# Kernel optimization log

Hardware: AMD Instinct MI355X
Metric: run time of the kernel (lower is better)

Reference implementation:

```python
import jax, jax.numpy as jnp
import numpy as np

N_QUBITS = 4
Q_DEPTH = 6
Q_DELTA = 0.01


def _conv1d(x, w, b):
    # x: (B, Cin, L), w: (Cout, Cin, 3), padding=1
    y = jax.lax.conv_general_dilated(x, w, window_strides=(1,), padding=[(1, 1)],
                                     dimension_numbers=('NCH', 'OIH', 'NCH'))
    return y + b[None, :, None]


def _maxpool2(x):
    B, C, L = x.shape
    return x.reshape(B, C, L // 2, 2).max(axis=-1)


def _take(state, i, axis):
    return jax.lax.index_in_dim(state, i, axis, keepdims=False)


def _apply_ry(state, theta, wire):
    # state: (B, 2, 2, 2, 2); theta: scalar (shared weight) or (B,) (per-sample)
    half = theta * 0.5
    c, s = jnp.cos(half), jnp.sin(half)
    if c.ndim == 1:  # per-sample angles -> broadcast over remaining qubit axes
        c = c.reshape(-1, 1, 1, 1)
        s = s.reshape(-1, 1, 1, 1)
    ax = wire + 1
    s0 = _take(state, 0, ax)
    s1 = _take(state, 1, ax)
    return jnp.stack([c * s0 - s * s1, s * s0 + c * s1], axis=ax)


def _apply_cnot(state, ctrl, tgt):
    cax, tax = ctrl + 1, tgt + 1
    a0 = jax.lax.slice_in_dim(state, 0, 1, axis=cax)
    a1 = jax.lax.slice_in_dim(state, 1, 2, axis=cax)
    return jnp.concatenate([a0, jnp.flip(a1, axis=tax)], axis=cax)


def _quantum_forward(q_in, q_params):
    # Batched 4-qubit state-vector simulation (PennyLane default.qubit semantics,
    # wire 0 = most significant -> axis wire+1 of (B,2,2,2,2) state).
    B = q_in.shape[0]
    # H layer on |0000> -> uniform amplitude 1/4
    state = jnp.full((B, 2, 2, 2, 2), 0.25, dtype=q_in.dtype)
    for w in range(N_QUBITS):
        state = _apply_ry(state, q_in[:, w], w)
    qw = q_params.reshape(Q_DEPTH, N_QUBITS)
    for k in range(Q_DEPTH):
        # entangling layer: CNOT(0,1), CNOT(2,3), then CNOT(1,2)
        state = _apply_cnot(state, 0, 1)
        state = _apply_cnot(state, 2, 3)
        state = _apply_cnot(state, 1, 2)
        for w in range(N_QUBITS):
            state = _apply_ry(state, qw[k, w], w)
    probs = state * state  # real amplitudes throughout (H as initial |+>^n, RY, CNOT)
    zs = [(_take(probs, 0, q + 1) - _take(probs, 1, q + 1)).sum(axis=(1, 2, 3))
          for q in range(N_QUBITS)]
    return jnp.stack(zs, axis=1)  # (B, 4) <Z_q>


def setup_inputs() -> dict:
    key = jax.random.key(0)
    ks = jax.random.split(key, 12)
    B, F = 32768, 64
    FLAT = 64 * (F // 4)  # 1024
    return {
        'x': jax.random.normal(ks[0], (B, F), jnp.float32),
        'conv1_w': jax.random.normal(ks[1], (32, 1, 3), jnp.float32) * 0.3,
        'conv1_b': jax.random.normal(ks[2], (32,), jnp.float32) * 0.05,
        'conv2_w': jax.random.normal(ks[3], (64, 32, 3), jnp.float32) * 0.05,
        'conv2_b': jax.random.normal(ks[4], (64,), jnp.float32) * 0.05,
        'fc_w': jax.random.normal(ks[5], (FLAT, 64), jnp.float32) * (1.0 / np.sqrt(FLAT)),
        'fc_b': jax.random.normal(ks[6], (64,), jnp.float32) * 0.05,
        'pre_w': jax.random.normal(ks[7], (64, N_QUBITS), jnp.float32) * 0.125,
        'pre_b': jax.random.normal(ks[8], (N_QUBITS,), jnp.float32) * 0.05,
        'q_params': Q_DELTA * jax.random.normal(ks[9], (Q_DEPTH * N_QUBITS,), jnp.float32),
        'post_w': jax.random.normal(ks[10], (N_QUBITS, 1), jnp.float32) * 0.5,
        'post_b': jax.random.normal(ks[11], (1,), jnp.float32) * 0.05,
    }


def reference(x, conv1_w, conv1_b, conv2_w, conv2_b, fc_w, fc_b,
              pre_w, pre_b, q_params, post_w, post_b):
    h = x[:, None, :]  # (B, 1, F)
    h = _maxpool2(jax.nn.relu(_conv1d(h, conv1_w, conv1_b)))   # (B, 32, F/2)
    h = _maxpool2(jax.nn.relu(_conv1d(h, conv2_w, conv2_b)))   # (B, 64, F/4)
    h = h.reshape(h.shape[0], -1)                              # (B, 1024)
    h = jax.nn.relu(h @ fc_w + fc_b)                           # (B, 64)
    q_in = jnp.tanh(h @ pre_w + pre_b) * (np.pi / 2.0)         # (B, 4)
    q_out = _quantum_forward(q_in, q_params)                   # (B, 4)
    return jax.nn.sigmoid(q_out @ post_w + post_b)             # (B, 1)
```

## Files before the change

### kernel.cpp

```cpp
#include <hip/hip_runtime.h>
#include <math.h>

typedef unsigned short u16;
typedef unsigned int u32;
typedef __attribute__((ext_vector_type(8))) short bf16x8;
typedef __attribute__((ext_vector_type(4))) float f32x4;
typedef __attribute__((ext_vector_type(2))) float f32x2;

__device__ __forceinline__ u16 f32_to_bf16(float f) {
    u32 u = __float_as_uint(f);
    u32 r = u + 0x7FFFu + ((u >> 16) & 1u);
    return (u16)(r >> 16);
}
__device__ __forceinline__ u32 pack2(u16 a, u16 b) { return (u32)a | ((u32)b << 16); }

__device__ __forceinline__ u32 cvt_pk_bf16(float a, float b) {
    u32 r;
    asm("v_cvt_pk_bf16_f32 %0, %1, %2" : "=v"(r) : "v"(a), "v"(b));
    return r;
}

__device__ __forceinline__ float fast_tanh(float x) {
    float e = __expf(2.f * x);
    return 1.f - 2.f / (e + 1.f);
}

template<int STRIDE>
__device__ __forceinline__ void ry_gate(float st[16], float theta) {
    float s, c;
    sincosf(theta * 0.5f, &s, &c);
#pragma unroll
    for (int i = 0; i < 16; ++i) {
        if (i & STRIDE) continue;
        float s0 = st[i], s1 = st[i | STRIDE];
        st[i]          = c * s0 - s * s1;
        st[i | STRIDE] = fmaf(s, s0, c * s1);
    }
}
template<int CS, int TS>
__device__ __forceinline__ void cnot_gate(float st[16]) {
#pragma unroll
    for (int i = 0; i < 16; ++i) {
        if ((i & CS) && !(i & TS)) {
            float tmp = st[i]; st[i] = st[i | TS]; st[i | TS] = tmp;
        }
    }
}

__global__ __launch_bounds__(256) void prep_kernel(
    const float* __restrict__ fcw, const float* __restrict__ w2,
    const float* __restrict__ qp,
    u16* __restrict__ whi, u16* __restrict__ w2b, float* __restrict__ Mg)
{
    __shared__ u16 T2[64][18];
    const int tid = threadIdx.x;
    const int b   = blockIdx.x;
    const int op  = b >> 2;
    const int q   = b & 3;

    {
        const int f  = tid & 63;
        const int wq = tid >> 6;
#pragma unroll
        for (int i = 0; i < 4; ++i) {
            const int ocl = wq * 4 + i;
            const int oc  = q * 16 + ocl;
            T2[f][ocl] = f32_to_bf16(fcw[(size_t)(oc * 16 + op) * 64 + f]);
        }
    }

    if (b < 24) {
        const int idx = b * 256 + tid;
        const int f  = idx / 96;
        const int j  = idx - f * 96;
        const int ic = j / 3, t = j - ic * 3;
        w2b[(t * 64 + f) * 32 + ic] = f32_to_bf16(w2[idx]);
    }

    __syncthreads();

    {
        const int f2 = tid >> 2;
        const int c0 = (tid & 3) * 4;
        u16 t0 = T2[f2][c0],     t1 = T2[f2][c0 + 1];
        u16 t2 = T2[f2][c0 + 2], t3 = T2[f2][c0 + 3];
        *(uint2*)(whi + (size_t)f2 * 1024 + op * 64 + q * 16 + c0) =
            make_uint2(pack2(t0, t1), pack2(t2, t3));
    }

    if (b == 0 && tid < 16) {
        const int j = tid;
        float st[16];
#pragma unroll
        for (int i = 0; i < 16; ++i) st[i] = (i == j) ? 1.f : 0.f;
        for (int k = 0; k < 6; ++k) {
            cnot_gate<8, 4>(st);
            cnot_gate<2, 1>(st);
            cnot_gate<4, 2>(st);
            ry_gate<8>(st, qp[k * 4 + 0]);
            ry_gate<4>(st, qp[k * 4 + 1]);
            ry_gate<2>(st, qp[k * 4 + 2]);
            ry_gate<1>(st, qp[k * 4 + 3]);
        }
#pragma unroll
        for (int i = 0; i < 16; ++i) Mg[i * 16 + j] = st[i];
    }
}

__global__ __launch_bounds__(512, 4) void fused_kernel(
    const float* __restrict__ x,
    const float* __restrict__ w1, const float* __restrict__ b1,
    const u16* __restrict__ w2b, const float* __restrict__ b2,
    const u16* __restrict__ whi,
    const float* __restrict__ fcb,
    const float* __restrict__ prew, const float* __restrict__ preb,
    const float* __restrict__ postw, const float* __restrict__ postb,
    const float* __restrict__ Mg,
    float* __restrict__ out)
{
    __shared__ __align__(16) u16 c1h[16 * 1368];
    __shared__ __align__(16) float part2[2 * 1024];
    __shared__ float prews[256];
    __shared__ float Ms[16][17];

    const int tid  = threadIdx.x;
    const int bs   = blockIdx.x * 16;
    const int wv   = tid >> 6, lane = tid & 63;
    const int lr   = lane & 15, lq = lane >> 4;

    const int s1 = tid >> 5;
    const int pp = tid & 31;
    const float* xb = x + (size_t)(bs + s1) * 64;
    const int j = 2 * pp;
    const float2 xv = *(const float2*)(xb + j);
    float x0 = xv.x, x1 = xv.y;

    bf16x8 af[3][4];
#pragma unroll
    for (int t = 0; t < 3; ++t)
#pragma unroll
        for (int mt = 0; mt < 4; ++mt)
            af[t][mt] = *(const bf16x8*)(w2b + (size_t)(t * 64 + mt * 16 + lr) * 32 + lq * 8);
    f32x4 bias2[4];
#pragma unroll
    for (int mt = 0; mt < 4; ++mt)
        bias2[mt] = *(const f32x4*)(b2 + mt * 16 + lq * 4);

    const int g  = wv & 3;
    const int hf = wv >> 2;
    const int n0 = g * 16;
    const float fcbv = (hf == 0) ? fcb[n0 + lr] : 0.f;

    if (tid < 256) {
        prews[tid] = prew[tid];
        Ms[tid >> 4][tid & 15] = Mg[tid];
    }

    float xm1 = __shfl_up(x1, 1);   if (pp == 0)  xm1 = 0.f;
    float xp2 = __shfl_down(x0, 1); if (pp == 31) xp2 = 0.f;

    {
        u16* sbase = c1h + s1 * 1368;
        if (pp == 0 || pp == 31) {
            uint4 z = make_uint4(0, 0, 0, 0);
            uint4* zr = (uint4*)(sbase + (pp == 0 ? 0 : 33) * 40);
            zr[0] = z; zr[1] = z; zr[2] = z; zr[3] = z;
        }
        const f32x2 A1 = {xm1, x0};
        const f32x2 A2 = {x0,  x1};
        const f32x2 A3 = {x1,  xp2};
        u32 row[16];
#pragma unroll
        for (int icp = 0; icp < 16; ++icp) {
            float v[2];
#pragma unroll
            for (int h2 = 0; h2 < 2; ++h2) {
                int ic = icp * 2 + h2;
                float wa = w1[ic * 3], wb = w1[ic * 3 + 1], wc = w1[ic * 3 + 2], bb = b1[ic];
                f32x2 Y = {bb, bb};
                Y += wa * A1;
                Y += wb * A2;
                Y += wc * A3;
                v[h2] = fmaxf(fmaxf(Y.x, Y.y), 0.f);
            }
            row[icp] = cvt_pk_bf16(v[0], v[1]);
        }
        uint4* d = (uint4*)(sbase + (1 + pp) * 40);
        d[0] = make_uint4(row[0],  row[1],  row[2],  row[3]);
        d[1] = make_uint4(row[4],  row[5],  row[6],  row[7]);
        d[2] = make_uint4(row[8],  row[9],  row[10], row[11]);
        d[3] = make_uint4(row[12], row[13], row[14], row[15]);
    }

#pragma unroll
    for (int nt = 0; nt < 4; ++nt) {
        const int s  = wv * 2 + (nt >> 1);
        const int qb = (nt & 1) * 16;
        const u16* bp = c1h + s * 1368 + (qb + lr) * 40 + lq * 8;
        bf16x8 bf0 = *(const bf16x8*)(bp);
        bf16x8 bf1 = *(const bf16x8*)(bp + 40);
        bf16x8 bf2 = *(const bf16x8*)(bp + 80);
        const int op = (qb + lr) >> 1;
#pragma unroll
        for (int mt = 0; mt < 4; ++mt) {
            f32x4 acc = __builtin_amdgcn_mfma_f32_16x16x32_bf16(af[0][mt], bf0, bias2[mt], 0, 0, 0);
            acc = __builtin_amdgcn_mfma_f32_16x16x32_bf16(af[1][mt], bf1, acc, 0, 0, 0);
            acc = __builtin_amdgcn_mfma_f32_16x16x32_bf16(af[2][mt], bf2, acc, 0, 0, 0);
            float p0 = fmaxf(fmaxf(acc[0], __shfl_xor(acc[0], 1)), 0.f);
            float p1 = fmaxf(fmaxf(acc[1], __shfl_xor(acc[1], 1)), 0.f);
            float p2 = fmaxf(fmaxf(acc[2], __shfl_xor(acc[2], 1)), 0.f);
            float p3 = fmaxf(fmaxf(acc[3], __shfl_xor(acc[3], 1)), 0.f);
            if (!(lane & 1)) {
                *(uint2*)(c1h + s * 1368 + op * 72 + mt * 16 + lq * 4) =
                    make_uint2(cvt_pk_bf16(p0, p1), cvt_pk_bf16(p2, p3));
            }
        }
    }
    __syncthreads();

    f32x4 accA = {0.f, 0.f, 0.f, 0.f};
    f32x4 accB = {0.f, 0.f, 0.f, 0.f};
    {
        const u16* ab0 = c1h + (size_t)lr * 1368 + lq * 8;
        const u16* bh0 = whi + (size_t)(n0 + lr) * 1024 + hf * 16 * 32 + lq * 8;
#pragma unroll
        for (int i = 0; i < 16; i += 2) {
            const int kcA = hf * 16 + i;
            const int kcB = kcA + 1;
            const int aoffA = (kcA >> 1) * 72 + (kcA & 1) * 32;
            const int aoffB = (kcB >> 1) * 72 + (kcB & 1) * 32;
            bf16x8 a0 = *(const bf16x8*)(ab0 + aoffA);
            bf16x8 a1 = *(const bf16x8*)(ab0 + aoffB);
            bf16x8 f0 = *(const bf16x8*)(bh0 + i * 32);
            bf16x8 f1 = *(const bf16x8*)(bh0 + (i + 1) * 32);
            accA = __builtin_amdgcn_mfma_f32_16x16x32_bf16(a0, f0, accA, 0, 0, 0);
            accB = __builtin_amdgcn_mfma_f32_16x16x32_bf16(a1, f1, accB, 0, 0, 0);
        }
    }
    f32x4 acc0 = accA + accB;
    acc0[0] += fcbv; acc0[1] += fcbv; acc0[2] += fcbv; acc0[3] += fcbv;
    *(f32x4*)(&part2[hf * 1024 + (n0 + lr) * 16 + lq * 4]) = acc0;
    __syncthreads();

    if (wv < 2) {
        const int L8 = lane & 7;
        const int s  = wv * 8 + (lane >> 3);

        float a0 = 0.f, a1 = 0.f, a2 = 0.f, a3 = 0.f;
#pragma unroll
        for (int i = 0; i < 8; ++i) {
            int ff = L8 * 8 + ((i + L8) & 7);
            float hx = fmaxf(part2[ff * 16 + s] + part2[1024 + ff * 16 + s], 0.f);
            float4 pw = *(const float4*)&prews[ff * 4];
            a0 = fmaf(hx, pw.x, a0);
            a1 = fmaf(hx, pw.y, a1);
            a2 = fmaf(hx, pw.z, a2);
            a3 = fmaf(hx, pw.w, a3);
        }
        a0 += __shfl_xor(a0, 1); a0 += __shfl_xor(a0, 2); a0 += __shfl_xor(a0, 4);
        a1 += __shfl_xor(a1, 1); a1 += __shfl_xor(a1, 2); a1 += __shfl_xor(a1, 4);
        a2 += __shfl_xor(a2, 1); a2 += __shfl_xor(a2, 2); a2 += __shfl_xor(a2, 4);
        a3 += __shfl_xor(a3, 1); a3 += __shfl_xor(a3, 2); a3 += __shfl_xor(a3, 4);

        const float HP = 1.5707963267948966f;
        float qin[4] = { fast_tanh(a0 + preb[0]) * HP, fast_tanh(a1 + preb[1]) * HP,
                         fast_tanh(a2 + preb[2]) * HP, fast_tanh(a3 + preb[3]) * HP };

        float va[4], vb[4];
        const float RS = 0.70710678118654752f;
#pragma unroll
        for (int w = 0; w < 4; ++w) {
            float sw, cw;
            __sincosf(qin[w] * 0.5f, &sw, &cw);
            va[w] = (cw - sw) * RS;
            vb[w] = (sw + cw) * RS;
        }
        float sv[16];
#pragma unroll
        for (int jj = 0; jj < 16; ++jj) {
            float t = (jj & 8) ? vb[0] : va[0];
            t *= (jj & 4) ? vb[1] : va[1];
            t *= (jj & 2) ? vb[2] : va[2];
            t *= (jj & 1) ? vb[3] : va[3];
            sv[jj] = t;
        }
        float z0 = 0.f, z1 = 0.f, z2 = 0.f, z3 = 0.f;
#pragma unroll
        for (int rr = 0; rr < 2; ++rr) {
            const int r = L8 * 2 + rr;
            float m = 0.f;
#pragma unroll
            for (int jj = 0; jj < 16; ++jj) m = fmaf(Ms[r][jj], sv[jj], m);
            float p = m * m;
            z0 += (r & 8) ? -p : p;
            z1 += (r & 4) ? -p : p;
            z2 += (r & 2) ? -p : p;
            z3 += (r & 1) ? -p : p;
        }
        z0 += __shfl_xor(z0, 1); z0 += __shfl_xor(z0, 2); z0 += __shfl_xor(z0, 4);
        z1 += __shfl_xor(z1, 1); z1 += __shfl_xor(z1, 2); z1 += __shfl_xor(z1, 4);
        z2 += __shfl_xor(z2, 1); z2 += __shfl_xor(z2, 2); z2 += __shfl_xor(z2, 4);
        z3 += __shfl_xor(z3, 1); z3 += __shfl_xor(z3, 2); z3 += __shfl_xor(z3, 4);

        if (L8 == 0) {
            float t = postb[0] + z0 * postw[0] + z1 * postw[1] + z2 * postw[2] + z3 * postw[3];
            out[bs + s] = 1.f / (1.f + __expf(-t));
        }
    }
}

extern "C" void kernel_launch(void* const* d_in, const int* in_sizes, int n_in,
                              void* d_out, int out_size, void* d_ws, size_t ws_size,
                              hipStream_t stream) {
    const float* x     = (const float*)d_in[0];
    const float* w1    = (const float*)d_in[1];
    const float* b1    = (const float*)d_in[2];
    const float* w2    = (const float*)d_in[3];
    const float* b2    = (const float*)d_in[4];
    const float* fcw   = (const float*)d_in[5];
    const float* fcb   = (const float*)d_in[6];
    const float* prew  = (const float*)d_in[7];
    const float* preb  = (const float*)d_in[8];
    const float* qp    = (const float*)d_in[9];
    const float* postw = (const float*)d_in[10];
    const float* postb = (const float*)d_in[11];
    float* out = (float*)d_out;

    u16*   fwhi = (u16*)d_ws;
    float* Mg   = (float*)((char*)d_ws + 131072);
    u16*   w2b  = (u16*)((char*)d_ws + 132096);

    const int B = in_sizes[0] / 64;

    prep_kernel<<<dim3(64), dim3(256), 0, stream>>>(fcw, w2, qp, fwhi, w2b, Mg);
    fused_kernel<<<dim3(B / 16), dim3(512), 0, stream>>>(x, w1, b1, w2b, b2,
                                                         fwhi, fcb, prew, preb,
                                                         postw, postb, Mg, out);
}
```

Baseline: 133.6 us.

## Process four 16-sample tiles per block with prefetch of next input tile

Each block now loops over four consecutive 16-sample tiles instead of one, and the grid shrinks to a quarter of its former size. The per-block setup (loading prew, the quantum matrix and fc bias) is paid once per four tiles. The next tile's input is prefetched into registers while the current tile is being computed. The cost is fewer resident blocks to hide latency and a serialised loop inside each block. The conv2 weight fragments are still reloaded on every iteration.

```diff
diff --git a/kernel.cpp b/kernel.cpp
--- a/kernel.cpp
+++ b/kernel.cpp
@@ -124,105 +124,110 @@
     __shared__ float Ms[16][17];
 
     const int tid  = threadIdx.x;
-    const int bs   = blockIdx.x * 16;
     const int wv   = tid >> 6, lane = tid & 63;
     const int lr   = lane & 15, lq = lane >> 4;
 
     const int s1 = tid >> 5;
     const int pp = tid & 31;
-    const float* xb = x + (size_t)(bs + s1) * 64;
-    const int j = 2 * pp;
-    const float2 xv = *(const float2*)(xb + j);
-    float x0 = xv.x, x1 = xv.y;
-
-    bf16x8 af[3][4];
-#pragma unroll
-    for (int t = 0; t < 3; ++t)
-#pragma unroll
-        for (int mt = 0; mt < 4; ++mt)
-            af[t][mt] = *(const bf16x8*)(w2b + (size_t)(t * 64 + mt * 16 + lr) * 32 + lq * 8);
-    f32x4 bias2[4];
-#pragma unroll
-    for (int mt = 0; mt < 4; ++mt)
-        bias2[mt] = *(const f32x4*)(b2 + mt * 16 + lq * 4);
+    const int j  = 2 * pp;
+    const float* xbase = x + (size_t)(blockIdx.x * 64 + s1) * 64;
+    float2 xv = *(const float2*)(xbase + j);
 
     const int g  = wv & 3;
     const int hf = wv >> 2;
     const int n0 = g * 16;
     const float fcbv = (hf == 0) ? fcb[n0 + lr] : 0.f;
+    const u16* ab0 = c1h + (size_t)lr * 1368 + lq * 8;
+    const u16* bh0 = whi + (size_t)(n0 + lr) * 1024 + hf * 16 * 32 + lq * 8;
 
     if (tid < 256) {
         prews[tid] = prew[tid];
         Ms[tid >> 4][tid & 15] = Mg[tid];
     }
 
-    float xm1 = __shfl_up(x1, 1);   if (pp == 0)  xm1 = 0.f;
-    float xp2 = __shfl_down(x0, 1); if (pp == 31) xp2 = 0.f;
-
-    {
-        u16* sbase = c1h + s1 * 1368;
-        if (pp == 0 || pp == 31) {
-            uint4 z = make_uint4(0, 0, 0, 0);
-            uint4* zr = (uint4*)(sbase + (pp == 0 ? 0 : 33) * 40);
-            zr[0] = z; zr[1] = z; zr[2] = z; zr[3] = z;
-        }
-        const f32x2 A1 = {xm1, x0};
-        const f32x2 A2 = {x0,  x1};
-        const f32x2 A3 = {x1,  xp2};
-        u32 row[16];
-#pragma unroll
-        for (int icp = 0; icp < 16; ++icp) {
-            float v[2];
-#pragma unroll
-            for (int h2 = 0; h2 < 2; ++h2) {
-                int ic = icp * 2 + h2;
-                float wa = w1[ic * 3], wb = w1[ic * 3 + 1], wc = w1[ic * 3 + 2], bb = b1[ic];
-                f32x2 Y = {bb, bb};
-                Y += wa * A1;
-                Y += wb * A2;
-                Y += wc * A3;
-                v[h2] = fmaxf(fmaxf(Y.x, Y.y), 0.f);
-            }
-            row[icp] = cvt_pk_bf16(v[0], v[1]);
-        }
-        uint4* d = (uint4*)(sbase + (1 + pp) * 40);
-        d[0] = make_uint4(row[0],  row[1],  row[2],  row[3]);
-        d[1] = make_uint4(row[4],  row[5],  row[6],  row[7]);
-        d[2] = make_uint4(row[8],  row[9],  row[10], row[11]);
-        d[3] = make_uint4(row[12], row[13], row[14], row[15]);
-    }
-
-#pragma unroll
-    for (int nt = 0; nt < 4; ++nt) {
-        const int s  = wv * 2 + (nt >> 1);
-        const int qb = (nt & 1) * 16;
-        const u16* bp = c1h + s * 1368 + (qb + lr) * 40 + lq * 8;
-        bf16x8 bf0 = *(const bf16x8*)(bp);
-        bf16x8 bf1 = *(const bf16x8*)(bp + 40);
-        bf16x8 bf2 = *(const bf16x8*)(bp + 80);
-        const int op = (qb + lr) >> 1;
-#pragma unroll
-        for (int mt = 0; mt < 4; ++mt) {
-            f32x4 acc = __builtin_amdgcn_mfma_f32_16x16x32_bf16(af[0][mt], bf0, bias2[mt], 0, 0, 0);
-            acc = __builtin_amdgcn_mfma_f32_16x16x32_bf16(af[1][mt], bf1, acc, 0, 0, 0);
-            acc = __builtin_amdgcn_mfma_f32_16x16x32_bf16(af[2][mt], bf2, acc, 0, 0, 0);
-            float p0 = fmaxf(fmaxf(acc[0], __shfl_xor(acc[0], 1)), 0.f);
-            float p1 = fmaxf(fmaxf(acc[1], __shfl_xor(acc[1], 1)), 0.f);
-            float p2 = fmaxf(fmaxf(acc[2], __shfl_xor(acc[2], 1)), 0.f);
-            float p3 = fmaxf(fmaxf(acc[3], __shfl_xor(acc[3], 1)), 0.f);
-            if (!(lane & 1)) {
-                *(uint2*)(c1h + s * 1368 + op * 72 + mt * 16 + lq * 4) =
-                    make_uint2(cvt_pk_bf16(p0, p1), cvt_pk_bf16(p2, p3));
-            }
-        }
-    }
-    __syncthreads();
-
-    f32x4 accA = {0.f, 0.f, 0.f, 0.f};
-    f32x4 accB = {0.f, 0.f, 0.f, 0.f};
-    {
-        const u16* ab0 = c1h + (size_t)lr * 1368 + lq * 8;
-        const u16* bh0 = whi + (size_t)(n0 + lr) * 1024 + hf * 16 * 32 + lq * 8;
+#pragma unroll 1
+    for (int t = 0; t < 4; ++t) {
+        const int bs = (blockIdx.x * 4 + t) * 16;
+
+        float2 xnext;
+        if (t < 3) xnext = *(const float2*)(xbase + (t + 1) * 1024 + j);
+
+        bf16x8 af[3][4];
+#pragma unroll
+        for (int tt = 0; tt < 3; ++tt)
+#pragma unroll
+            for (int mt = 0; mt < 4; ++mt)
+                af[tt][mt] = *(const bf16x8*)(w2b + (size_t)(tt * 64 + mt * 16 + lr) * 32 + lq * 8);
+        f32x4 bias2[4];
+#pragma unroll
+        for (int mt = 0; mt < 4; ++mt)
+            bias2[mt] = *(const f32x4*)(b2 + mt * 16 + lq * 4);
+
+        float x0 = xv.x, x1 = xv.y;
+        float xm1 = __shfl_up(x1, 1);   if (pp == 0)  xm1 = 0.f;
+        float xp2 = __shfl_down(x0, 1); if (pp == 31) xp2 = 0.f;
+
+        {
+            u16* sbase = c1h + s1 * 1368;
+            if (pp == 0 || pp == 31) {
+                uint4 z = make_uint4(0, 0, 0, 0);
+                uint4* zr = (uint4*)(sbase + (pp == 0 ? 0 : 33) * 40);
+                zr[0] = z; zr[1] = z; zr[2] = z; zr[3] = z;
+            }
+            const f32x2 A1 = {xm1, x0};
+            const f32x2 A2 = {x0,  x1};
+            const f32x2 A3 = {x1,  xp2};
+            u32 row[16];
+#pragma unroll
+            for (int icp = 0; icp < 16; ++icp) {
+                float v[2];
+#pragma unroll
+                for (int h2 = 0; h2 < 2; ++h2) {
+                    int ic = icp * 2 + h2;
+                    float wa = w1[ic * 3], wb = w1[ic * 3 + 1], wc = w1[ic * 3 + 2], bb = b1[ic];
+                    f32x2 Y = {bb, bb};
+                    Y += wa * A1;
+                    Y += wb * A2;
+                    Y += wc * A3;
+                    v[h2] = fmaxf(fmaxf(Y.x, Y.y), 0.f);
+                }
+                row[icp] = cvt_pk_bf16(v[0], v[1]);
+            }
+            uint4* d = (uint4*)(sbase + (1 + pp) * 40);
+            d[0] = make_uint4(row[0],  row[1],  row[2],  row[3]);
+            d[1] = make_uint4(row[4],  row[5],  row[6],  row[7]);
+            d[2] = make_uint4(row[8],  row[9],  row[10], row[11]);
+            d[3] = make_uint4(row[12], row[13], row[14], row[15]);
+        }
+
+#pragma unroll
+        for (int nt = 0; nt < 4; ++nt) {
+            const int s  = wv * 2 + (nt >> 1);
+            const int qb = (nt & 1) * 16;
+            const u16* bp = c1h + s * 1368 + (qb + lr) * 40 + lq * 8;
+            bf16x8 bf0 = *(const bf16x8*)(bp);
+            bf16x8 bf1 = *(const bf16x8*)(bp + 40);
+            bf16x8 bf2 = *(const bf16x8*)(bp + 80);
+            const int op = (qb + lr) >> 1;
+#pragma unroll
+            for (int mt = 0; mt < 4; ++mt) {
+                f32x4 acc = __builtin_amdgcn_mfma_f32_16x16x32_bf16(af[0][mt], bf0, bias2[mt], 0, 0, 0);
+                acc = __builtin_amdgcn_mfma_f32_16x16x32_bf16(af[1][mt], bf1, acc, 0, 0, 0);
+                acc = __builtin_amdgcn_mfma_f32_16x16x32_bf16(af[2][mt], bf2, acc, 0, 0, 0);
+                float p0 = fmaxf(fmaxf(acc[0], __shfl_xor(acc[0], 1)), 0.f);
+                float p1 = fmaxf(fmaxf(acc[1], __shfl_xor(acc[1], 1)), 0.f);
+                float p2 = fmaxf(fmaxf(acc[2], __shfl_xor(acc[2], 1)), 0.f);
+                float p3 = fmaxf(fmaxf(acc[3], __shfl_xor(acc[3], 1)), 0.f);
+                if (!(lane & 1)) {
+                    *(uint2*)(c1h + s * 1368 + op * 72 + mt * 16 + lq * 4) =
+                        make_uint2(cvt_pk_bf16(p0, p1), cvt_pk_bf16(p2, p3));
+                }
+            }
+        }
+        __syncthreads();
+
+        f32x4 accA = {0.f, 0.f, 0.f, 0.f};
+        f32x4 accB = {0.f, 0.f, 0.f, 0.f};
 #pragma unroll
         for (int i = 0; i < 16; i += 2) {
             const int kcA = hf * 16 + i;
@@ -236,76 +241,78 @@
             accA = __builtin_amdgcn_mfma_f32_16x16x32_bf16(a0, f0, accA, 0, 0, 0);
             accB = __builtin_amdgcn_mfma_f32_16x16x32_bf16(a1, f1, accB, 0, 0, 0);
         }
-    }
-    f32x4 acc0 = accA + accB;
-    acc0[0] += fcbv; acc0[1] += fcbv; acc0[2] += fcbv; acc0[3] += fcbv;
-    *(f32x4*)(&part2[hf * 1024 + (n0 + lr) * 16 + lq * 4]) = acc0;
-    __syncthreads();
-
-    if (wv < 2) {
-        const int L8 = lane & 7;
-        const int s  = wv * 8 + (lane >> 3);
-
-        float a0 = 0.f, a1 = 0.f, a2 = 0.f, a3 = 0.f;
-#pragma unroll
-        for (int i = 0; i < 8; ++i) {
-            int ff = L8 * 8 + ((i + L8) & 7);
-            float hx = fmaxf(part2[ff * 16 + s] + part2[1024 + ff * 16 + s], 0.f);
-            float4 pw = *(const float4*)&prews[ff * 4];
-            a0 = fmaf(hx, pw.x, a0);
-            a1 = fmaf(hx, pw.y, a1);
-            a2 = fmaf(hx, pw.z, a2);
-            a3 = fmaf(hx, pw.w, a3);
-        }
-        a0 += __shfl_xor(a0, 1); a0 += __shfl_xor(a0, 2); a0 += __shfl_xor(a0, 4);
-        a1 += __shfl_xor(a1, 1); a1 += __shfl_xor(a1, 2); a1 += __shfl_xor(a1, 4);
-        a2 += __shfl_xor(a2, 1); a2 += __shfl_xor(a2, 2); a2 += __shfl_xor(a2, 4);
-        a3 += __shfl_xor(a3, 1); a3 += __shfl_xor(a3, 2); a3 += __shfl_xor(a3, 4);
-
-        const float HP = 1.5707963267948966f;
-        float qin[4] = { fast_tanh(a0 + preb[0]) * HP, fast_tanh(a1 + preb[1]) * HP,
-                         fast_tanh(a2 + preb[2]) * HP, fast_tanh(a3 + preb[3]) * HP };
-
-        float va[4], vb[4];
-        const float RS = 0.70710678118654752f;
-#pragma unroll
-        for (int w = 0; w < 4; ++w) {
-            float sw, cw;
-            __sincosf(qin[w] * 0.5f, &sw, &cw);
-            va[w] = (cw - sw) * RS;
-            vb[w] = (sw + cw) * RS;
-        }
-        float sv[16];
-#pragma unroll
-        for (int jj = 0; jj < 16; ++jj) {
-            float t = (jj & 8) ? vb[0] : va[0];
-            t *= (jj & 4) ? vb[1] : va[1];
-            t *= (jj & 2) ? vb[2] : va[2];
-            t *= (jj & 1) ? vb[3] : va[3];
-            sv[jj] = t;
-        }
-        float z0 = 0.f, z1 = 0.f, z2 = 0.f, z3 = 0.f;
-#pragma unroll
-        for (int rr = 0; rr < 2; ++rr) {
-            const int r = L8 * 2 + rr;
-            float m = 0.f;
-#pragma unroll
-            for (int jj = 0; jj < 16; ++jj) m = fmaf(Ms[r][jj], sv[jj], m);
-            float p = m * m;
-            z0 += (r & 8) ? -p : p;
-            z1 += (r & 4) ? -p : p;
-            z2 += (r & 2) ? -p : p;
-            z3 += (r & 1) ? -p : p;
-        }
-        z0 += __shfl_xor(z0, 1); z0 += __shfl_xor(z0, 2); z0 += __shfl_xor(z0, 4);
-        z1 += __shfl_xor(z1, 1); z1 += __shfl_xor(z1, 2); z1 += __shfl_xor(z1, 4);
-        z2 += __shfl_xor(z2, 1); z2 += __shfl_xor(z2, 2); z2 += __shfl_xor(z2, 4);
-        z3 += __shfl_xor(z3, 1); z3 += __shfl_xor(z3, 2); z3 += __shfl_xor(z3, 4);
-
-        if (L8 == 0) {
-            float t = postb[0] + z0 * postw[0] + z1 * postw[1] + z2 * postw[2] + z3 * postw[3];
-            out[bs + s] = 1.f / (1.f + __expf(-t));
-        }
+        f32x4 acc0 = accA + accB;
+        acc0[0] += fcbv; acc0[1] += fcbv; acc0[2] += fcbv; acc0[3] += fcbv;
+        *(f32x4*)(&part2[hf * 1024 + (n0 + lr) * 16 + lq * 4]) = acc0;
+        __syncthreads();
+
+        if (wv < 2) {
+            const int L8 = lane & 7;
+            const int s  = wv * 8 + (lane >> 3);
+
+            float a0 = 0.f, a1 = 0.f, a2 = 0.f, a3 = 0.f;
+#pragma unroll
+            for (int i = 0; i < 8; ++i) {
+                int ff = L8 * 8 + ((i + L8) & 7);
+                float hx = fmaxf(part2[ff * 16 + s] + part2[1024 + ff * 16 + s], 0.f);
+                float4 pw = *(const float4*)&prews[ff * 4];
+                a0 = fmaf(hx, pw.x, a0);
+                a1 = fmaf(hx, pw.y, a1);
+                a2 = fmaf(hx, pw.z, a2);
+                a3 = fmaf(hx, pw.w, a3);
+            }
+            a0 += __shfl_xor(a0, 1); a0 += __shfl_xor(a0, 2); a0 += __shfl_xor(a0, 4);
+            a1 += __shfl_xor(a1, 1); a1 += __shfl_xor(a1, 2); a1 += __shfl_xor(a1, 4);
+            a2 += __shfl_xor(a2, 1); a2 += __shfl_xor(a2, 2); a2 += __shfl_xor(a2, 4);
+            a3 += __shfl_xor(a3, 1); a3 += __shfl_xor(a3, 2); a3 += __shfl_xor(a3, 4);
+
+            const float HP = 1.5707963267948966f;
+            float qin[4] = { fast_tanh(a0 + preb[0]) * HP, fast_tanh(a1 + preb[1]) * HP,
+                             fast_tanh(a2 + preb[2]) * HP, fast_tanh(a3 + preb[3]) * HP };
+
+            float va[4], vb[4];
+            const float RS = 0.70710678118654752f;
+#pragma unroll
+            for (int w = 0; w < 4; ++w) {
+                float sw, cw;
+                __sincosf(qin[w] * 0.5f, &sw, &cw);
+                va[w] = (cw - sw) * RS;
+                vb[w] = (sw + cw) * RS;
+            }
+            float sv[16];
+#pragma unroll
+            for (int jj = 0; jj < 16; ++jj) {
+                float tt = (jj & 8) ? vb[0] : va[0];
+                tt *= (jj & 4) ? vb[1] : va[1];
+                tt *= (jj & 2) ? vb[2] : va[2];
+                tt *= (jj & 1) ? vb[3] : va[3];
+                sv[jj] = tt;
+            }
+            float z0 = 0.f, z1 = 0.f, z2 = 0.f, z3 = 0.f;
+#pragma unroll
+            for (int rr = 0; rr < 2; ++rr) {
+                const int r = L8 * 2 + rr;
+                float m = 0.f;
+#pragma unroll
+                for (int jj = 0; jj < 16; ++jj) m = fmaf(Ms[r][jj], sv[jj], m);
+                float p = m * m;
+                z0 += (r & 8) ? -p : p;
+                z1 += (r & 4) ? -p : p;
+                z2 += (r & 2) ? -p : p;
+                z3 += (r & 1) ? -p : p;
+            }
+            z0 += __shfl_xor(z0, 1); z0 += __shfl_xor(z0, 2); z0 += __shfl_xor(z0, 4);
+            z1 += __shfl_xor(z1, 1); z1 += __shfl_xor(z1, 2); z1 += __shfl_xor(z1, 4);
+            z2 += __shfl_xor(z2, 1); z2 += __shfl_xor(z2, 2); z2 += __shfl_xor(z2, 4);
+            z3 += __shfl_xor(z3, 1); z3 += __shfl_xor(z3, 2); z3 += __shfl_xor(z3, 4);
+
+            if (L8 == 0) {
+                float tt = postb[0] + z0 * postw[0] + z1 * postw[1] + z2 * postw[2] + z3 * postw[3];
+                out[bs + s] = 1.f / (1.f + __expf(-tt));
+            }
+        }
+
+        xv = xnext;
     }
 }
 
@@ -333,7 +340,7 @@
     const int B = in_sizes[0] / 64;
 
     prep_kernel<<<dim3(64), dim3(256), 0, stream>>>(fcw, w2, qp, fwhi, w2b, Mg);
-    fused_kernel<<<dim3(B / 16), dim3(512), 0, stream>>>(x, w1, b1, w2b, b2,
+    fused_kernel<<<dim3(B / 64), dim3(512), 0, stream>>>(x, w1, b1, w2b, b2,
                                                          fwhi, fcb, prew, preb,
                                                          postw, postb, Mg, out);
 }
```

Measured after the change: 140.7 us. +5.3%, slower.
